# Optimization experiments

Measured on AMD Instinct MI355X. Metric: run time of the kernel, lower is better.

## Reference

```python
import jax, jax.numpy as jnp
import numpy as np

N_NODES = 10000
N_EDGES = 70000
H = 128
L = 15  # message_passing_num
NODE_IN = 11  # 2 frame dims + 9 one-hot node types
EDGE_IN = 3
LN_EPS = 1e-5


def _mlp(x, W1, b1, W2, b2):
    return jax.nn.relu(x @ W1 + b1) @ W2 + b2


def _mlp_ln(x, W1, b1, W2, b2, g, b):
    h = _mlp(x, W1, b1, W2, b2)
    mu = jnp.mean(h, axis=-1, keepdims=True)
    var = jnp.var(h, axis=-1, keepdims=True)
    return (h - mu) * jax.lax.rsqrt(var + LN_EPS) * g + b


def setup_inputs() -> dict:
    key = jax.random.key(0)
    ks = iter(jax.random.split(key, 40))
    rn = lambda shp, s: (jax.random.normal(next(ks), shp, jnp.float32) * s)
    inp = {
        "node_type": jax.random.randint(next(ks), (N_NODES,), 0, 9, jnp.int32),
        "edge_index": jax.random.randint(next(ks), (2, N_EDGES), 0, N_NODES, jnp.int32),
        "frames": jax.random.normal(next(ks), (N_NODES, 2), jnp.float32),
        "edge_feats": jax.random.normal(next(ks), (N_EDGES, EDGE_IN), jnp.float32),
        "node_norm_mean": jax.random.normal(next(ks), (NODE_IN,), jnp.float32) * 0.1,
        "node_norm_std": jax.random.uniform(next(ks), (NODE_IN,), jnp.float32) + 0.5,
        "out_norm_mean": jax.random.normal(next(ks), (2,), jnp.float32) * 0.1,
        "out_norm_std": jax.random.uniform(next(ks), (2,), jnp.float32) + 0.5,
        # encoder node MLP (11 -> 128 -> 128, LayerNorm)
        "enc_nW1": rn((NODE_IN, H), NODE_IN ** -0.5), "enc_nb1": jnp.zeros((H,)),
        "enc_nW2": rn((H, H), H ** -0.5), "enc_nb2": jnp.zeros((H,)),
        "enc_nlng": jnp.ones((H,)), "enc_nlnb": jnp.zeros((H,)),
        # encoder edge MLP (3 -> 128 -> 128, LayerNorm)
        "enc_eW1": rn((EDGE_IN, H), EDGE_IN ** -0.5), "enc_eb1": jnp.zeros((H,)),
        "enc_eW2": rn((H, H), H ** -0.5), "enc_eb2": jnp.zeros((H,)),
        "enc_elng": jnp.ones((H,)), "enc_elnb": jnp.zeros((H,)),
        # L GNN blocks, stacked. Edge MLP: 3H -> H -> H (+LN); Node MLP: 2H -> H -> H (+LN)
        "eb_W1": rn((L, 3 * H, H), (3 * H) ** -0.5), "eb_b1": jnp.zeros((L, H)),
        "eb_W2": rn((L, H, H), H ** -0.5), "eb_b2": jnp.zeros((L, H)),
        "eb_lng": jnp.ones((L, H)), "eb_lnb": jnp.zeros((L, H)),
        "nb_W1": rn((L, 2 * H, H), (2 * H) ** -0.5), "nb_b1": jnp.zeros((L, H)),
        "nb_W2": rn((L, H, H), H ** -0.5), "nb_b2": jnp.zeros((L, H)),
        "nb_lng": jnp.ones((L, H)), "nb_lnb": jnp.zeros((L, H)),
        # decoder MLP (128 -> 128 -> 2, no LayerNorm)
        "dec_W1": rn((H, H), H ** -0.5), "dec_b1": jnp.zeros((H,)),
        "dec_W2": rn((H, 2), H ** -0.5), "dec_b2": jnp.zeros((2,)),
    }
    return inp


def reference(node_type, edge_index, frames, edge_feats,
              node_norm_mean, node_norm_std, out_norm_mean, out_norm_std,
              enc_nW1, enc_nb1, enc_nW2, enc_nb2, enc_nlng, enc_nlnb,
              enc_eW1, enc_eb1, enc_eW2, enc_eb2, enc_elng, enc_elnb,
              eb_W1, eb_b1, eb_W2, eb_b2, eb_lng, eb_lnb,
              nb_W1, nb_b1, nb_W2, nb_b2, nb_lng, nb_lnb,
              dec_W1, dec_b1, dec_W2, dec_b2):
    n_nodes = frames.shape[0]
    senders, receivers = edge_index[0], edge_index[1]

    # update_node_attr: concat(frames, one_hot(type, 9)) then normalize (eval mode)
    one_hot = jax.nn.one_hot(node_type, 9, dtype=frames.dtype)
    node_feats = jnp.concatenate([frames, one_hot], axis=1)  # [N, 11]
    node_attr = (node_feats - node_norm_mean) / node_norm_std

    # Encoder
    x = _mlp_ln(node_attr, enc_nW1, enc_nb1, enc_nW2, enc_nb2, enc_nlng, enc_nlnb)   # [N, H]
    e = _mlp_ln(edge_feats, enc_eW1, enc_eb1, enc_eW2, enc_eb2, enc_elng, enc_elnb)  # [E, H]

    # Processor: L residual GNN blocks (EdgeBlock then NodeBlock)
    def block(carry, p):
        x, e = carry
        (eW1, eb1, eW2, eb2, eg, ebn, nW1, nb1, nW2, nb2, ng, nbn) = p
        e_in = jnp.concatenate([x[senders], x[receivers], e], axis=-1)  # [E, 3H]
        e_new = _mlp_ln(e_in, eW1, eb1, eW2, eb2, eg, ebn)              # [E, H]
        agg = jax.ops.segment_sum(e_new, receivers, num_segments=n_nodes)  # [N, H]
        x_new = _mlp_ln(jnp.concatenate([x, agg], axis=-1), nW1, nb1, nW2, nb2, ng, nbn)
        return (x + x_new, e + e_new), None

    (x, e), _ = jax.lax.scan(
        block, (x, e),
        (eb_W1, eb_b1, eb_W2, eb_b2, eb_lng, eb_lnb,
         nb_W1, nb_b1, nb_W2, nb_b2, nb_lng, nb_lnb))

    # Decoder (no LayerNorm) + inverse output normalization (eval path)
    decoded = _mlp(x, dec_W1, dec_b1, dec_W2, dec_b2)  # [N, 2]
    velocity_update = decoded * out_norm_std + out_norm_mean
    return frames + velocity_update
```

## Files before the change

kernel.cpp:

```cpp
#include <hip/hip_runtime.h>
#include <hip/hip_bf16.h>

#define N_NODES 10000
#define N_EDGES 70000
#define NPAD 10112
#define EPAD 70016
#define H 128
#define NLAYERS 15
constexpr float LN_EPS = 1e-5f;

typedef __attribute__((ext_vector_type(8))) short short8;
typedef __attribute__((ext_vector_type(4))) float f32x4;

__device__ __forceinline__ float bf2f(unsigned int ulo16) {
    return __uint_as_float(ulo16 << 16);
}
__device__ __forceinline__ unsigned short f2bf(float f) {
    unsigned int x = __float_as_uint(f);
    x += 0x7fffu + ((x >> 16) & 1u);
    return (unsigned short)(x >> 16);
}

__global__ void prep_node(const int* __restrict__ nt, const float* __restrict__ frames,
                          const float* __restrict__ nm, const float* __restrict__ ns,
                          unsigned short* __restrict__ a16b) {
    int i = blockIdx.x * blockDim.x + threadIdx.x;
    if (i >= NPAD * 32) return;
    int n = i >> 5, k = i & 31;
    float v = 0.f;
    if (n < N_NODES && k < 11) {
        float raw = (k < 2) ? frames[n * 2 + k] : ((nt[n] == (k - 2)) ? 1.f : 0.f);
        v = (raw - nm[k]) / ns[k];
    }
    a16b[i] = f2bf(v);
}

__global__ void prep_edge(const float* __restrict__ ef, unsigned short* __restrict__ a4b) {
    int i = blockIdx.x * blockDim.x + threadIdx.x;
    if (i >= EPAD * 32) return;
    int e = i >> 5, k = i & 31;
    float v = (e < N_EDGES && k < 3) ? ef[e * 3 + k] : 0.f;
    a4b[i] = f2bf(v);
}

__global__ void transpose_w_frag(const float* __restrict__ w, unsigned short* __restrict__ wt,
                                 int Kr, int Kp, int nmat) {
    __shared__ float T[32][33];
    int nkt = Kp / 32;
    int bid = blockIdx.x;
    int m = bid / (nkt * 4);
    int rest = bid % (nkt * 4);
    int kt = rest / 4, ct = rest % 4;
    int t = threadIdx.x;
    int tc = t & 31, tr = t >> 5;
#pragma unroll
    for (int rr = 0; rr < 4; ++rr) {
        int k = kt * 32 + tr + rr * 8;
        int c = ct * 32 + tc;
        T[tr + rr * 8][tc] = (k < Kr) ? w[((size_t)m * Kr + k) * H + c] : 0.f;
    }
    __syncthreads();
#pragma unroll
    for (int rr = 0; rr < 4; ++rr) {
        int c = ct * 32 + tr + rr * 8;
        int k = kt * 32 + tc;
        size_t fidx = ((((size_t)m * nkt + (k >> 5)) * 8 + (c >> 4)) * 64
                       + ((k >> 3) & 3) * 16 + (c & 15)) * 8 + (k & 7);
        wt[fidx] = f2bf(T[tc][tr + rr * 8]);
    }
}

__global__ void hist_kernel(const int* __restrict__ rcv, int* __restrict__ counts) {
    int j = blockIdx.x * blockDim.x + threadIdx.x;
    if (j < N_EDGES) atomicAdd(&counts[rcv[j]], 1);
}

__global__ void scan_kernel(const int* __restrict__ counts, int* __restrict__ starts) {
    __shared__ int part[1024];
    const int CH = 10;
    int t = threadIdx.x;
    int base = t * CH;
    int loc[CH];
    int s = 0;
#pragma unroll
    for (int i = 0; i < CH; i++) {
        int idx = base + i;
        int c = (idx < N_NODES) ? counts[idx] : 0;
        loc[i] = s;
        s += c;
    }
    part[t] = s;
    __syncthreads();
    for (int off = 1; off < 1024; off <<= 1) {
        int v = (t >= off) ? part[t - off] : 0;
        __syncthreads();
        part[t] += v;
        __syncthreads();
    }
    int pre = (t > 0) ? part[t - 1] : 0;
#pragma unroll
    for (int i = 0; i < CH; i++) {
        int idx = base + i;
        if (idx < N_NODES) starts[idx] = pre + loc[i];
    }
}

__global__ void scatter_kernel(const int* __restrict__ rcv, const int* __restrict__ starts,
                               int* __restrict__ cursor, int* __restrict__ esorted) {
    int j = blockIdx.x * blockDim.x + threadIdx.x;
    if (j >= N_EDGES) return;
    int r = rcv[j];
    int p = starts[r] + atomicAdd(&cursor[r], 1);
    esorted[p] = j;
}

__global__ void agg_kernel(const unsigned short* __restrict__ enew,
                           const int* __restrict__ esorted,
                           const int* __restrict__ starts,
                           const int* __restrict__ counts,
                           unsigned short* __restrict__ aggb) {
    int n = blockIdx.x * 16 + (threadIdx.x >> 4);
    int l = threadIdx.x & 15;
    if (n >= N_NODES) return;
    float a[8];
#pragma unroll
    for (int q = 0; q < 8; ++q) a[q] = 0.f;
    int s0 = starts[n], cnt = counts[n];
    for (int j = 0; j < cnt; ++j) {
        int e = esorted[s0 + j];
        uint4 v = *reinterpret_cast<const uint4*>(enew + (size_t)e * H + l * 8);
        a[0] += bf2f(v.x & 0xffffu); a[1] += bf2f(v.x >> 16);
        a[2] += bf2f(v.y & 0xffffu); a[3] += bf2f(v.y >> 16);
        a[4] += bf2f(v.z & 0xffffu); a[5] += bf2f(v.z >> 16);
        a[6] += bf2f(v.w & 0xffffu); a[7] += bf2f(v.w >> 16);
    }
    uint4 o;
    o.x = (unsigned int)f2bf(a[0]) | ((unsigned int)f2bf(a[1]) << 16);
    o.y = (unsigned int)f2bf(a[2]) | ((unsigned int)f2bf(a[3]) << 16);
    o.z = (unsigned int)f2bf(a[4]) | ((unsigned int)f2bf(a[5]) << 16);
    o.w = (unsigned int)f2bf(a[6]) | ((unsigned int)f2bf(a[7]) << 16);
    *reinterpret_cast<uint4*>(aggb + (size_t)n * H + l * 8) = o;
}

template <int K1, int AMODE, int EPI, int RW>
__launch_bounds__(256)
__global__ void mlp_wave(const unsigned short* __restrict__ A,
                         const unsigned short* __restrict__ Xb,
                         const unsigned short* __restrict__ Eb,
                         const unsigned short* __restrict__ Gb,
                         const int* __restrict__ snd,
                         const int* __restrict__ rcv,
                         const unsigned short* __restrict__ Bt1,
                         const float* __restrict__ bias1,
                         const unsigned short* __restrict__ Bt2,
                         const float* __restrict__ bias2,
                         const float* __restrict__ lng,
                         const float* __restrict__ lnb,
                         unsigned short* __restrict__ out_bf,
                         float* __restrict__ out_fp,
                         unsigned short* __restrict__ enew_bf,
                         int nrows) {
    constexpr int SH = H + 8;
    __shared__ __attribute__((aligned(16))) unsigned short Hs[4 * 16 * RW * SH];

    const int tid = threadIdx.x;
    const int wave = tid >> 6;
    const int lane = tid & 63;
    const int l15 = lane & 15;
    const int lhi = lane >> 4;
    const int wrow0 = (blockIdx.x * 4 + wave) * (16 * RW);
    unsigned short* Hw = Hs + wave * (16 * RW) * SH;

    const unsigned short* pS[RW];
    const unsigned short* pR[RW];
    const unsigned short* pE[RW];
#pragma unroll
    for (int i = 0; i < RW; ++i) {
        int grow = wrow0 + i * 16 + l15;
        if (AMODE == 0) {
            pS[i] = A + (size_t)grow * K1;
        } else if (AMODE == 1) {
            int e = (grow < nrows) ? grow : (nrows - 1);
            pS[i] = Xb + (size_t)snd[e] * H;
            pR[i] = Xb + (size_t)rcv[e] * H;
            pE[i] = Eb + (size_t)grow * H;
        } else {
            pS[i] = Xb + (size_t)grow * H;
            pR[i] = Gb + (size_t)grow * H;
        }
    }

    f32x4 acc[RW][8];
#pragma unroll
    for (int i = 0; i < RW; i++)
#pragma unroll
        for (int j = 0; j < 8; j++) acc[i][j] = (f32x4){0.f, 0.f, 0.f, 0.f};

#pragma unroll 4
    for (int kc = 0; kc < K1; kc += 32) {
        short8 af[RW];
#pragma unroll
        for (int i = 0; i < RW; ++i) {
            const unsigned short* s;
            if (AMODE == 0)      s = pS[i] + kc;
            else if (AMODE == 1) s = (kc < H) ? pS[i] + kc
                                 : (kc < 2 * H) ? pR[i] + (kc - H)
                                 : pE[i] + (kc - 2 * H);
            else                 s = (kc < H) ? pS[i] + kc : pR[i] + (kc - H);
            af[i] = *reinterpret_cast<const short8*>(s + lhi * 8);
        }
        const unsigned short* bbase = Bt1 + ((size_t)(kc >> 5) * 8) * 512 + lane * 8;
#pragma unroll
        for (int j = 0; j < 8; ++j) {
            short8 bfr = *reinterpret_cast<const short8*>(bbase + j * 512);
#pragma unroll
            for (int i = 0; i < RW; ++i)
                acc[i][j] = __builtin_amdgcn_mfma_f32_16x16x32_bf16(af[i], bfr, acc[i][j], 0, 0, 0);
        }
    }

    {
        float b1v[8];
#pragma unroll
        for (int j = 0; j < 8; ++j) b1v[j] = bias1[j * 16 + l15];
#pragma unroll
        for (int i = 0; i < RW; ++i)
#pragma unroll
            for (int r = 0; r < 4; ++r) {
                int rl = i * 16 + lhi * 4 + r;
#pragma unroll
                for (int j = 0; j < 8; ++j) {
                    float v = acc[i][j][r] + b1v[j];
                    Hw[rl * SH + j * 16 + l15] = f2bf(v > 0.f ? v : 0.f);
                }
            }
    }

#pragma unroll
    for (int i = 0; i < RW; i++)
#pragma unroll
        for (int j = 0; j < 8; j++) acc[i][j] = (f32x4){0.f, 0.f, 0.f, 0.f};

#pragma unroll
    for (int kc = 0; kc < H; kc += 32) {
        short8 af[RW];
#pragma unroll
        for (int i = 0; i < RW; ++i)
            af[i] = *reinterpret_cast<const short8*>(&Hw[(i * 16 + l15) * SH + kc + lhi * 8]);
        const unsigned short* bbase = Bt2 + ((size_t)(kc >> 5) * 8) * 512 + lane * 8;
#pragma unroll
        for (int j = 0; j < 8; ++j) {
            short8 bfr = *reinterpret_cast<const short8*>(bbase + j * 512);
#pragma unroll
            for (int i = 0; i < RW; ++i)
                acc[i][j] = __builtin_amdgcn_mfma_f32_16x16x32_bf16(af[i], bfr, acc[i][j], 0, 0, 0);
        }
    }

    float bv[8], gv[8], lv[8];
#pragma unroll
    for (int j = 0; j < 8; ++j) {
        bv[j] = bias2[j * 16 + l15];
        gv[j] = lng[j * 16 + l15];
        lv[j] = lnb[j * 16 + l15];
    }

#pragma unroll
    for (int i = 0; i < RW; ++i) {
#pragma unroll
        for (int r = 0; r < 4; ++r) {
            int row = wrow0 + i * 16 + lhi * 4 + r;
            float v[8];
            float s = 0.f, s2 = 0.f;
#pragma unroll
            for (int j = 0; j < 8; ++j) {
                v[j] = acc[i][j][r] + bv[j];
                s += v[j];
                s2 += v[j] * v[j];
            }
#pragma unroll
            for (int m = 1; m < 16; m <<= 1) {
                s += __shfl_xor(s, m);
                s2 += __shfl_xor(s2, m);
            }
            float mean = s * (1.f / 128.f);
            float var = s2 * (1.f / 128.f) - mean * mean;
            float rstd = rsqrtf(var + LN_EPS);
            if (row < nrows) {
#pragma unroll
                for (int j = 0; j < 8; ++j) {
                    float o = (v[j] - mean) * rstd * gv[j] + lv[j];
                    size_t off = (size_t)row * H + j * 16 + l15;
                    if (EPI == 1) {
                        out_fp[off] = o;
                        out_bf[off] = f2bf(o);
                    } else if (EPI == 2) {
                        float nx = out_fp[off] + o;
                        out_fp[off] = nx;
                        out_bf[off] = f2bf(nx);
                    } else {
                        float ne = out_fp[off] + o;
                        out_fp[off] = ne;
                        out_bf[off] = f2bf(ne);
                        enew_bf[off] = f2bf(o);
                    }
                }
            }
        }
    }
}

__global__ void decoder_kernel(const float* __restrict__ x,
                               const float* __restrict__ frames,
                               const float* __restrict__ W1, const float* __restrict__ b1,
                               const float* __restrict__ W2, const float* __restrict__ b2,
                               const float* __restrict__ omean, const float* __restrict__ ostd,
                               float* __restrict__ outp) {
    __shared__ float xr[H];
    __shared__ float hr[H];
    __shared__ float red[2][2];
    int n = blockIdx.x;
    int t = threadIdx.x;
    xr[t] = x[n * H + t];
    __syncthreads();
    float acc = 0.f;
#pragma unroll 8
    for (int k = 0; k < H; k++) acc += xr[k] * W1[k * H + t];
    hr[t] = fmaxf(acc + b1[t], 0.f);
    __syncthreads();
    float p0 = hr[t] * W2[t * 2 + 0];
    float p1 = hr[t] * W2[t * 2 + 1];
#pragma unroll
    for (int m = 1; m < 64; m <<= 1) {
        p0 += __shfl_xor(p0, m);
        p1 += __shfl_xor(p1, m);
    }
    if ((t & 63) == 0) { red[t >> 6][0] = p0; red[t >> 6][1] = p1; }
    __syncthreads();
    if (t < 2) {
        float d = red[0][t] + red[1][t] + b2[t];
        outp[n * 2 + t] = frames[n * 2 + t] + d * ostd[t] + omean[t];
    }
}

extern "C" void kernel_launch(void* const* d_in, const int* in_sizes, int n_in,
                              void* d_out, int out_size, void* d_ws, size_t ws_size,
                              hipStream_t stream) {
    (void)in_sizes; (void)n_in; (void)out_size; (void)ws_size;
    const int*   node_type  = (const int*)  d_in[0];
    const int*   edge_index = (const int*)  d_in[1];
    const float* frames     = (const float*)d_in[2];
    const float* edge_feats = (const float*)d_in[3];
    const float* nmean      = (const float*)d_in[4];
    const float* nstd       = (const float*)d_in[5];
    const float* omean      = (const float*)d_in[6];
    const float* ostd       = (const float*)d_in[7];
    const float* enc_nW1    = (const float*)d_in[8];
    const float* enc_nb1    = (const float*)d_in[9];
    const float* enc_nW2    = (const float*)d_in[10];
    const float* enc_nb2    = (const float*)d_in[11];
    const float* enc_nlng   = (const float*)d_in[12];
    const float* enc_nlnb   = (const float*)d_in[13];
    const float* enc_eW1    = (const float*)d_in[14];
    const float* enc_eb1    = (const float*)d_in[15];
    const float* enc_eW2    = (const float*)d_in[16];
    const float* enc_eb2    = (const float*)d_in[17];
    const float* enc_elng   = (const float*)d_in[18];
    const float* enc_elnb   = (const float*)d_in[19];
    const float* eb_W1      = (const float*)d_in[20];
    const float* eb_b1      = (const float*)d_in[21];
    const float* eb_W2      = (const float*)d_in[22];
    const float* eb_b2      = (const float*)d_in[23];
    const float* eb_g       = (const float*)d_in[24];
    const float* eb_bn      = (const float*)d_in[25];
    const float* nb_W1      = (const float*)d_in[26];
    const float* nb_b1      = (const float*)d_in[27];
    const float* nb_W2      = (const float*)d_in[28];
    const float* nb_b2      = (const float*)d_in[29];
    const float* nb_g       = (const float*)d_in[30];
    const float* nb_bn      = (const float*)d_in[31];
    const float* dec_W1     = (const float*)d_in[32];
    const float* dec_b1     = (const float*)d_in[33];
    const float* dec_W2     = (const float*)d_in[34];
    const float* dec_b2     = (const float*)d_in[35];

    const int* snd = edge_index;
    const int* rcv = edge_index + N_EDGES;

    char* p = (char*)d_ws;
    auto alloc = [&](size_t bytes) {
        void* r = (void*)p;
        p += (bytes + 255) & ~(size_t)255;
        return r;
    };
    float* x_fp  = (float*)alloc((size_t)NPAD * H * 4);
    float* e_fp  = (float*)alloc((size_t)EPAD * H * 4);
    unsigned short* x_bf   = (unsigned short*)alloc((size_t)NPAD * H * 2);
    unsigned short* e_bf   = (unsigned short*)alloc((size_t)EPAD * H * 2);
    unsigned short* enew   = (unsigned short*)alloc((size_t)EPAD * H * 2);
    unsigned short* agg_bf = (unsigned short*)alloc((size_t)NPAD * H * 2);
    unsigned short* a16b   = (unsigned short*)alloc((size_t)NPAD * 32 * 2);
    unsigned short* a4b    = (unsigned short*)alloc((size_t)EPAD * 32 * 2);
    unsigned short* wt_en1 = (unsigned short*)alloc((size_t)128 * 32 * 2);
    unsigned short* wt_ee1 = (unsigned short*)alloc((size_t)128 * 32 * 2);
    unsigned short* wt_en2 = (unsigned short*)alloc((size_t)128 * 128 * 2);
    unsigned short* wt_ee2 = (unsigned short*)alloc((size_t)128 * 128 * 2);
    unsigned short* wt_eb1 = (unsigned short*)alloc((size_t)NLAYERS * 128 * 384 * 2);
    unsigned short* wt_eb2 = (unsigned short*)alloc((size_t)NLAYERS * 128 * 128 * 2);
    unsigned short* wt_nb1 = (unsigned short*)alloc((size_t)NLAYERS * 128 * 256 * 2);
    unsigned short* wt_nb2 = (unsigned short*)alloc((size_t)NLAYERS * 128 * 128 * 2);
    int* counts  = (int*)alloc((size_t)N_NODES * 4);
    int* starts  = (int*)alloc((size_t)N_NODES * 4);
    int* cursor  = (int*)alloc((size_t)N_NODES * 4);
    int* esorted = (int*)alloc((size_t)N_EDGES * 4);

    prep_node<<<(NPAD * 32 + 255) / 256, 256, 0, stream>>>(node_type, frames, nmean, nstd, a16b);
    prep_edge<<<(EPAD * 32 + 255) / 256, 256, 0, stream>>>(edge_feats, a4b);
    auto tw = [&](const float* w, unsigned short* wt, int Kr, int Kp, int nmat) {
        int blocks = nmat * (Kp / 32) * 4;
        transpose_w_frag<<<blocks, 256, 0, stream>>>(w, wt, Kr, Kp, nmat);
    };
    tw(enc_nW1, wt_en1, 11, 32, 1);
    tw(enc_eW1, wt_ee1, 3, 32, 1);
    tw(enc_nW2, wt_en2, 128, 128, 1);
    tw(enc_eW2, wt_ee2, 128, 128, 1);
    tw(eb_W1, wt_eb1, 384, 384, NLAYERS);
    tw(eb_W2, wt_eb2, 128, 128, NLAYERS);
    tw(nb_W1, wt_nb1, 256, 256, NLAYERS);
    tw(nb_W2, wt_nb2, 128, 128, NLAYERS);

    hipMemsetAsync(counts, 0, (size_t)N_NODES * 4, stream);
    hipMemsetAsync(cursor, 0, (size_t)N_NODES * 4, stream);
    hist_kernel<<<(N_EDGES + 255) / 256, 256, 0, stream>>>(rcv, counts);
    scan_kernel<<<1, 1024, 0, stream>>>(counts, starts);
    scatter_kernel<<<(N_EDGES + 255) / 256, 256, 0, stream>>>(rcv, starts, cursor, esorted);

    const int gE = EPAD / 128;
    const int gN = NPAD / 64;
    const unsigned short* nu_ = nullptr;
    const int* ni_ = nullptr;
    unsigned short* nm_ = nullptr;

    mlp_wave<32, 0, 1, 1><<<gN, 256, 0, stream>>>(a16b, nu_, nu_, nu_, ni_, ni_,
        wt_en1, enc_nb1, wt_en2, enc_nb2, enc_nlng, enc_nlnb,
        x_bf, x_fp, nm_, N_NODES);
    mlp_wave<32, 0, 1, 2><<<gE, 256, 0, stream>>>(a4b, nu_, nu_, nu_, ni_, ni_,
        wt_ee1, enc_eb1, wt_ee2, enc_eb2, enc_elng, enc_elnb,
        e_bf, e_fp, nm_, N_EDGES);

    for (int l = 0; l < NLAYERS; ++l) {
        mlp_wave<384, 1, 3, 2><<<gE, 256, 0, stream>>>(nu_, x_bf, e_bf, nu_, snd, rcv,
            wt_eb1 + (size_t)l * 128 * 384, eb_b1 + l * H,
            wt_eb2 + (size_t)l * 128 * 128, eb_b2 + l * H, eb_g + l * H, eb_bn + l * H,
            e_bf, e_fp, enew, N_EDGES);
        agg_kernel<<<(N_NODES + 15) / 16, 256, 0, stream>>>(enew, esorted, starts, counts, agg_bf);
        mlp_wave<256, 2, 2, 1><<<gN, 256, 0, stream>>>(nu_, x_bf, nu_, agg_bf, ni_, ni_,
            wt_nb1 + (size_t)l * 128 * 256, nb_b1 + l * H,
            wt_nb2 + (size_t)l * 128 * 128, nb_b2 + l * H, nb_g + l * H, nb_bn + l * H,
            x_bf, x_fp, nm_, N_NODES);
    }

    decoder_kernel<<<N_NODES, 128, 0, stream>>>(x_fp, frames, dec_W1, dec_b1, dec_W2, dec_b2,
                                                omean, ostd, (float*)d_out);
}
```

Before: 1.418 ms.

## Store edges in receiver-sorted order and shrink MLP tiles for occupancy

Edges are permuted once into receiver-sorted order: edge features, sender and receiver indices are reordered up front, so the per-layer edge state is held in sorted order. Aggregation then reads each node's edges contiguously instead of gathering through the esorted index. The MLP kernel also gains a wave-count template parameter, with smaller per-block row tiles (RW=1, more blocks) to raise parallelism. Extra setup kernels add one-time cost, and smaller tiles reduce weight reuse per block. Final outputs are per-node, so correctness does not depend on edge order.

```diff
diff --git a/kernel.cpp b/kernel.cpp
--- a/kernel.cpp
+++ b/kernel.cpp
@@ -35,12 +35,24 @@
     a16b[i] = f2bf(v);
 }
 
-__global__ void prep_edge(const float* __restrict__ ef, unsigned short* __restrict__ a4b) {
+__global__ void prep_edge_sorted(const float* __restrict__ ef, const int* __restrict__ esorted,
+                                 unsigned short* __restrict__ a4b) {
     int i = blockIdx.x * blockDim.x + threadIdx.x;
     if (i >= EPAD * 32) return;
-    int e = i >> 5, k = i & 31;
-    float v = (e < N_EDGES && k < 3) ? ef[e * 3 + k] : 0.f;
+    int p = i >> 5, k = i & 31;
+    float v = 0.f;
+    if (p < N_EDGES && k < 3) v = ef[(size_t)esorted[p] * 3 + k];
     a4b[i] = f2bf(v);
+}
+
+__global__ void permute_idx(const int* __restrict__ snd, const int* __restrict__ rcv,
+                            const int* __restrict__ esorted,
+                            int* __restrict__ sndP, int* __restrict__ rcvP) {
+    int p = blockIdx.x * blockDim.x + threadIdx.x;
+    if (p >= N_EDGES) return;
+    int j = esorted[p];
+    sndP[p] = snd[j];
+    rcvP[p] = rcv[j];
 }
 
 __global__ void transpose_w_frag(const float* __restrict__ w, unsigned short* __restrict__ wt,
@@ -115,7 +127,6 @@
 }
 
 __global__ void agg_kernel(const unsigned short* __restrict__ enew,
-                           const int* __restrict__ esorted,
                            const int* __restrict__ starts,
                            const int* __restrict__ counts,
                            unsigned short* __restrict__ aggb) {
@@ -126,9 +137,9 @@
 #pragma unroll
     for (int q = 0; q < 8; ++q) a[q] = 0.f;
     int s0 = starts[n], cnt = counts[n];
+    const unsigned short* base = enew + (size_t)s0 * H + l * 8;
     for (int j = 0; j < cnt; ++j) {
-        int e = esorted[s0 + j];
-        uint4 v = *reinterpret_cast<const uint4*>(enew + (size_t)e * H + l * 8);
+        uint4 v = *reinterpret_cast<const uint4*>(base + (size_t)j * H);
         a[0] += bf2f(v.x & 0xffffu); a[1] += bf2f(v.x >> 16);
         a[2] += bf2f(v.y & 0xffffu); a[3] += bf2f(v.y >> 16);
         a[4] += bf2f(v.z & 0xffffu); a[5] += bf2f(v.z >> 16);
@@ -142,8 +153,8 @@
     *reinterpret_cast<uint4*>(aggb + (size_t)n * H + l * 8) = o;
 }
 
-template <int K1, int AMODE, int EPI, int RW>
-__launch_bounds__(256)
+template <int K1, int AMODE, int EPI, int RW, int NW>
+__launch_bounds__(NW * 64)
 __global__ void mlp_wave(const unsigned short* __restrict__ A,
                          const unsigned short* __restrict__ Xb,
                          const unsigned short* __restrict__ Eb,
@@ -161,14 +172,14 @@
                          unsigned short* __restrict__ enew_bf,
                          int nrows) {
     constexpr int SH = H + 8;
-    __shared__ __attribute__((aligned(16))) unsigned short Hs[4 * 16 * RW * SH];
+    __shared__ __attribute__((aligned(16))) unsigned short Hs[NW * 16 * RW * SH];
 
     const int tid = threadIdx.x;
     const int wave = tid >> 6;
     const int lane = tid & 63;
     const int l15 = lane & 15;
     const int lhi = lane >> 4;
-    const int wrow0 = (blockIdx.x * 4 + wave) * (16 * RW);
+    const int wrow0 = (blockIdx.x * NW + wave) * (16 * RW);
     unsigned short* Hw = Hs + wave * (16 * RW) * SH;
 
     const unsigned short* pS[RW];
@@ -183,10 +194,11 @@
             int e = (grow < nrows) ? grow : (nrows - 1);
             pS[i] = Xb + (size_t)snd[e] * H;
             pR[i] = Xb + (size_t)rcv[e] * H;
-            pE[i] = Eb + (size_t)grow * H;
+            pE[i] = Eb + (size_t)e * H;
         } else {
-            pS[i] = Xb + (size_t)grow * H;
-            pR[i] = Gb + (size_t)grow * H;
+            int e = (grow < nrows) ? grow : (nrows - 1);
+            pS[i] = Xb + (size_t)e * H;
+            pR[i] = Gb + (size_t)e * H;
         }
     }
 
@@ -413,9 +425,18 @@
     int* starts  = (int*)alloc((size_t)N_NODES * 4);
     int* cursor  = (int*)alloc((size_t)N_NODES * 4);
     int* esorted = (int*)alloc((size_t)N_EDGES * 4);
+    int* sndP    = (int*)alloc((size_t)N_EDGES * 4);
+    int* rcvP    = (int*)alloc((size_t)N_EDGES * 4);
+
+    hipMemsetAsync(counts, 0, (size_t)N_NODES * 4, stream);
+    hipMemsetAsync(cursor, 0, (size_t)N_NODES * 4, stream);
+    hist_kernel<<<(N_EDGES + 255) / 256, 256, 0, stream>>>(rcv, counts);
+    scan_kernel<<<1, 1024, 0, stream>>>(counts, starts);
+    scatter_kernel<<<(N_EDGES + 255) / 256, 256, 0, stream>>>(rcv, starts, cursor, esorted);
+    permute_idx<<<(N_EDGES + 255) / 256, 256, 0, stream>>>(snd, rcv, esorted, sndP, rcvP);
 
     prep_node<<<(NPAD * 32 + 255) / 256, 256, 0, stream>>>(node_type, frames, nmean, nstd, a16b);
-    prep_edge<<<(EPAD * 32 + 255) / 256, 256, 0, stream>>>(edge_feats, a4b);
+    prep_edge_sorted<<<(EPAD * 32 + 255) / 256, 256, 0, stream>>>(edge_feats, esorted, a4b);
     auto tw = [&](const float* w, unsigned short* wt, int Kr, int Kp, int nmat) {
         int blocks = nmat * (Kp / 32) * 4;
         transpose_w_frag<<<blocks, 256, 0, stream>>>(w, wt, Kr, Kp, nmat);
@@ -429,32 +450,26 @@
     tw(nb_W1, wt_nb1, 256, 256, NLAYERS);
     tw(nb_W2, wt_nb2, 128, 128, NLAYERS);
 
-    hipMemsetAsync(counts, 0, (size_t)N_NODES * 4, stream);
-    hipMemsetAsync(cursor, 0, (size_t)N_NODES * 4, stream);
-    hist_kernel<<<(N_EDGES + 255) / 256, 256, 0, stream>>>(rcv, counts);
-    scan_kernel<<<1, 1024, 0, stream>>>(counts, starts);
-    scatter_kernel<<<(N_EDGES + 255) / 256, 256, 0, stream>>>(rcv, starts, cursor, esorted);
-
-    const int gE = EPAD / 128;
-    const int gN = NPAD / 64;
+    const int gE = EPAD / 64;
+    const int gN = NPAD / 32;
     const unsigned short* nu_ = nullptr;
     const int* ni_ = nullptr;
     unsigned short* nm_ = nullptr;
 
-    mlp_wave<32, 0, 1, 1><<<gN, 256, 0, stream>>>(a16b, nu_, nu_, nu_, ni_, ni_,
+    mlp_wave<32, 0, 1, 1, 2><<<gN, 128, 0, stream>>>(a16b, nu_, nu_, nu_, ni_, ni_,
         wt_en1, enc_nb1, wt_en2, enc_nb2, enc_nlng, enc_nlnb,
         x_bf, x_fp, nm_, N_NODES);
-    mlp_wave<32, 0, 1, 2><<<gE, 256, 0, stream>>>(a4b, nu_, nu_, nu_, ni_, ni_,
+    mlp_wave<32, 0, 1, 1, 4><<<gE, 256, 0, stream>>>(a4b, nu_, nu_, nu_, ni_, ni_,
         wt_ee1, enc_eb1, wt_ee2, enc_eb2, enc_elng, enc_elnb,
         e_bf, e_fp, nm_, N_EDGES);
 
     for (int l = 0; l < NLAYERS; ++l) {
-        mlp_wave<384, 1, 3, 2><<<gE, 256, 0, stream>>>(nu_, x_bf, e_bf, nu_, snd, rcv,
+        mlp_wave<384, 1, 3, 1, 4><<<gE, 256, 0, stream>>>(nu_, x_bf, e_bf, nu_, sndP, rcvP,
             wt_eb1 + (size_t)l * 128 * 384, eb_b1 + l * H,
             wt_eb2 + (size_t)l * 128 * 128, eb_b2 + l * H, eb_g + l * H, eb_bn + l * H,
             e_bf, e_fp, enew, N_EDGES);
-        agg_kernel<<<(N_NODES + 15) / 16, 256, 0, stream>>>(enew, esorted, starts, counts, agg_bf);
-        mlp_wave<256, 2, 2, 1><<<gN, 256, 0, stream>>>(nu_, x_bf, nu_, agg_bf, ni_, ni_,
+        agg_kernel<<<(N_NODES + 15) / 16, 256, 0, stream>>>(enew, starts, counts, agg_bf);
+        mlp_wave<256, 2, 2, 1, 2><<<gN, 128, 0, stream>>>(nu_, x_bf, nu_, agg_bf, ni_, ni_,
             wt_nb1 + (size_t)l * 128 * 256, nb_b1 + l * H,
             wt_nb2 + (size_t)l * 128 * 128, nb_b2 + l * H, nb_g + l * H, nb_bn + l * H,
             x_bf, x_fp, nm_, N_NODES);
```

Result: slower. 1.636 ms (+15.3%).
